# Kernel tuning notes

Measured on AMD Instinct MI355X. Metric: run time of the kernel, lower is better.

The kernel has to match this reference:

```python
import jax, jax.numpy as jnp
import numpy as np

NQ, NKV, D = 16, 2, 128
GROUPS = NQ // NKV
HID = 2048
SCALE = D ** -0.5
SLIDING_WINDOW = 32768
USE_WINDOW = True  # layer_idx 0 < max_window_layers 28
ROPE_THETA = 1e6


def rotate_half(x):
    h = x.shape[-1] // 2
    return jnp.concatenate([-x[..., h:], x[..., :h]], axis=-1)


def setup_inputs() -> dict:
    key = jax.random.key(0)
    ks = jax.random.split(key, 8)
    B, T = 1, 4096
    x = jax.random.normal(ks[0], (B, T, HID), dtype=jnp.float32)
    # Real RoPE tables (cos/sin over [T, D])
    inv_freq = 1.0 / (ROPE_THETA ** (np.arange(0, D, 2, dtype=np.float64) / D))
    freqs = np.outer(np.arange(T, dtype=np.float64), inv_freq)
    emb = np.concatenate([freqs, freqs], axis=-1)  # [T, D]
    cos = jnp.asarray(np.cos(emb), dtype=jnp.float32)
    sin = jnp.asarray(np.sin(emb), dtype=jnp.float32)
    std = 0.02
    wq = jax.random.normal(ks[1], (NQ * D, HID), dtype=jnp.float32) * std
    bq = jax.random.normal(ks[2], (NQ * D,), dtype=jnp.float32) * std
    wk = jax.random.normal(ks[3], (NKV * D, HID), dtype=jnp.float32) * std
    bk = jax.random.normal(ks[4], (NKV * D,), dtype=jnp.float32) * std
    wv = jax.random.normal(ks[5], (NKV * D, HID), dtype=jnp.float32) * std
    bv = jax.random.normal(ks[6], (NKV * D,), dtype=jnp.float32) * std
    wo = jax.random.normal(ks[7], (HID, NQ * D), dtype=jnp.float32) * std
    return {"x": x, "cos": cos, "sin": sin, "wq": wq, "bq": bq,
            "wk": wk, "bk": bk, "wv": wv, "bv": bv, "wo": wo}


def reference(x, cos, sin, wq, bq, wk, bk, wv, bv, wo):
    B, T, _ = x.shape
    # Projections -> [B, heads, T, D]
    q = (x @ wq.T + bq).reshape(B, T, NQ, D).transpose(0, 2, 1, 3)
    k = (x @ wk.T + bk).reshape(B, T, NKV, D).transpose(0, 2, 1, 3)
    v = (x @ wv.T + bv).reshape(B, T, NKV, D).transpose(0, 2, 1, 3)
    # RoPE
    c = cos[:T][None, None]  # [1,1,T,D]
    s = sin[:T][None, None]
    q = q * c + rotate_half(q) * s
    k = k * c + rotate_half(k) * s
    S = k.shape[2]  # no kv_cache -> S == T
    # GQA: group q heads over kv heads instead of repeat_interleave (same math)
    qg = q.reshape(B, NKV, GROUPS, T, D)
    attn = jnp.einsum('bkgtd,bksd->bkgts', qg, k) * SCALE  # [B,nkv,g,T,S]
    row = jnp.arange(T)[:, None]
    col = jnp.arange(S)[None, :]
    mask = jnp.where(col > row + (S - T), -jnp.inf, 0.0).astype(x.dtype)
    if USE_WINDOW and S > SLIDING_WINDOW:  # static shapes -> ok under jit
        mask = jnp.where(col < S - SLIDING_WINDOW, -jnp.inf, mask)
    attn = jax.nn.softmax(attn + mask[None, None, None], axis=-1)
    out = jnp.einsum('bkgts,bksd->bkgtd', attn, v)  # [B,nkv,g,T,D]
    out = out.reshape(B, NQ, T, D).transpose(0, 2, 1, 3).reshape(B, T, NQ * D)
    return out @ wo.T
```

## Files before the change

kernel.cpp:

```cpp
#include <hip/hip_runtime.h>
#include <hip/hip_bf16.h>
#include <stdint.h>

#define T_SEQ 4096
#define HID   2048
#define NQH   16
#define NKVH  2
#define DH    128
#define NQKV  2560
#define SCALE 0.08838834764831845f
#define QK_PRESCALE (0.08838834764831845f * 1.4426950408889634f)

typedef unsigned short u16;
typedef __attribute__((ext_vector_type(8))) short bf16x8;
typedef __attribute__((ext_vector_type(4))) float f32x4;

#define MFMA(a, b, c) __builtin_amdgcn_mfma_f32_16x16x32_bf16(a, b, c, 0, 0, 0)

static __device__ __forceinline__ u16 f2bf(float f) {
    union { float f; uint32_t u; } v; v.f = f;
    uint32_t r = v.u + 0x7fffu + ((v.u >> 16) & 1u);
    return (u16)(r >> 16);
}
static __device__ __forceinline__ float bf2f(u16 u) {
    union { uint32_t u; float f; } v; v.u = ((uint32_t)u) << 16;
    return v.f;
}

static __device__ __forceinline__ void gload_lds16(const void* g, void* l) {
    __builtin_amdgcn_global_load_lds((const __attribute__((address_space(1))) uint32_t*)g,
                                     (__attribute__((address_space(3))) uint32_t*)l,
                                     16, 0, 0);
}

__global__ void k_cvt_all(const float4* __restrict__ x,  const float4* __restrict__ wq,
                          const float4* __restrict__ wk, const float4* __restrict__ wv,
                          const float4* __restrict__ wo,
                          u16* __restrict__ x_bf, u16* __restrict__ wqkv_bf,
                          u16* __restrict__ wo_bf) {
    const int i = blockIdx.x * 256 + threadIdx.x;
    const float4* src; u16* dst; int off;
    if (i < 2097152)      { src = x;  dst = x_bf;              off = i; }
    else if (i < 3145728) { src = wq; dst = wqkv_bf;           off = i - 2097152; }
    else if (i < 3276800) { src = wk; dst = wqkv_bf + 4194304; off = i - 3145728; }
    else if (i < 3407872) { src = wv; dst = wqkv_bf + 4718592; off = i - 3276800; }
    else                  { src = wo; dst = wo_bf;             off = i - 3407872; }
    const float4 v = src[off];
    const uint64_t o = (uint64_t)f2bf(v.x) | ((uint64_t)f2bf(v.y) << 16) |
                       ((uint64_t)f2bf(v.z) << 32) | ((uint64_t)f2bf(v.w) << 48);
    *(uint64_t*)(dst + (size_t)off * 4) = o;
}

__global__ void k_bias(const float* __restrict__ bq, const float* __restrict__ bk,
                       const float* __restrict__ bv, float* __restrict__ out) {
    int i = blockIdx.x * 256 + threadIdx.x;
    float v = (i < 2048) ? bq[i] : (i < 2304 ? bk[i - 2048] : bv[i - 2304]);
    out[i] = v;
}

template <int OUT_BF16>
__global__ __launch_bounds__(256, 2) void k_gemm_bt(const u16* __restrict__ A,
                                                    const u16* __restrict__ B,
                                                    const float* __restrict__ bias,
                                                    void* __restrict__ Cout,
                                                    int M, int N, int K) {
    __shared__ u16 As[128 * 32];
    __shared__ u16 Bs[128 * 32];
    const int tid  = threadIdx.x;
    const int lane = tid & 63, w = tid >> 6;
    const int wr = w >> 1, wc = w & 1;
    const int lrow = lane & 15, lgrp = lane >> 4;
    const int m0 = blockIdx.x * 128, n0 = blockIdx.y * 128;

    f32x4 acc[4][4] = {};
    const int arow = tid >> 2, acol = (tid & 3) * 8;
    const u16* Abase = A + (size_t)(m0 + arow) * K + acol;
    const u16* Bbase = B + (size_t)(n0 + arow) * K + acol;

    for (int kk = 0; kk < K; kk += 32) {
        gload_lds16(Abase + kk,                   &As[tid * 8]);
        gload_lds16(Abase + kk + (size_t)64 * K,  &As[2048 + tid * 8]);
        gload_lds16(Bbase + kk,                   &Bs[tid * 8]);
        gload_lds16(Bbase + kk + (size_t)64 * K,  &Bs[2048 + tid * 8]);
        __syncthreads();
        bf16x8 af[4], bfv[4];
#pragma unroll
        for (int mb = 0; mb < 4; ++mb)
            af[mb] = *(const bf16x8*)&As[(wr * 64 + mb * 16 + lrow) * 32 + lgrp * 8];
#pragma unroll
        for (int nb = 0; nb < 4; ++nb)
            bfv[nb] = *(const bf16x8*)&Bs[(wc * 64 + nb * 16 + lrow) * 32 + lgrp * 8];
#pragma unroll
        for (int mb = 0; mb < 4; ++mb)
#pragma unroll
            for (int nb = 0; nb < 4; ++nb)
                acc[mb][nb] = MFMA(af[mb], bfv[nb], acc[mb][nb]);
        __syncthreads();
    }
#pragma unroll
    for (int mb = 0; mb < 4; ++mb)
#pragma unroll
        for (int nb = 0; nb < 4; ++nb) {
            const int col = n0 + wc * 64 + nb * 16 + lrow;
            const float bv_ = bias ? bias[col] : 0.f;
#pragma unroll
            for (int r = 0; r < 4; ++r) {
                const int row = m0 + wr * 64 + mb * 16 + lgrp * 4 + r;
                const float v = acc[mb][nb][r] + bv_;
                if (OUT_BF16) ((u16*)Cout)[(size_t)row * N + col] = f2bf(v);
                else          ((float*)Cout)[(size_t)row * N + col] = v;
            }
        }
}

__global__ void k_rope(const u16* __restrict__ qkv, const float* __restrict__ cosb,
                       const float* __restrict__ sinb, u16* __restrict__ Q,
                       u16* __restrict__ Kd, u16* __restrict__ VT) {
    const int n = blockIdx.x * 256 + threadIdx.x;
    const int t = blockIdx.y;
    const u16* row = qkv + (size_t)t * NQKV;
    if (n < 2304) {
        const int d = n & 127;
        const float x = bf2f(row[n]);
        const float p = bf2f(row[(d < 64) ? n + 64 : n - 64]);
        const float c = cosb[t * DH + d], s = sinb[t * DH + d];
        float val = (d < 64) ? (x * c - p * s) : (x * c + p * s);
        if (n < 2048) {
            const int h = n >> 7;
            Q[((size_t)h * T_SEQ + t) * DH + d] = f2bf(val * QK_PRESCALE);
        } else {
            const int kh = (n - 2048) >> 7;
            const int u = (d >> 3) ^ (t & 7);
            Kd[((size_t)kh * T_SEQ + t) * DH + u * 8 + (d & 7)] = f2bf(val);
        }
    } else {
        const int nv = n - 2304;
        const int kh = nv >> 7, d = nv & 127;
        const int kappa = t & 63;
        const int c = (kappa & 15) * 4 + (kappa >> 4);
        const int u = (c >> 3) ^ (d & 7);
        VT[((size_t)kh * DH + d) * T_SEQ + (t & ~63) + u * 8 + (c & 7)] = row[n];
    }
}

__global__ __launch_bounds__(256, 2) void k_attn(const u16* __restrict__ Q,
                                                 const u16* __restrict__ Kg,
                                                 const u16* __restrict__ VT,
                                                 u16* __restrict__ O) {
    __shared__ u16 Ks[2][64 * 128];
    __shared__ u16 VTs[64 * 128];
    __shared__ __align__(16) u16 Pb[4][16][72];
    const int tid  = threadIdx.x;
    const int lane = tid & 63, w = tid >> 6;
    const int lrow = lane & 15, lgrp = lane >> 4;
    const int g = blockIdx.x;
    const int h = g & 15, pp = g >> 4;
    const int kvh = h >> 3;

    const u16* Kbase = Kg + (size_t)kvh * T_SEQ * DH;
    const u16* Vbase = VT + (size_t)kvh * DH * T_SEQ;

    auto STAGE_K = [&](int buf, int it) {
        const u16* kg = Kbase + (size_t)(it * 64 + (tid >> 4)) * DH + (tid & 15) * 8;
#pragma unroll
        for (int c = 0; c < 4; ++c)
            gload_lds16(kg + (size_t)c * 16 * DH, &Ks[buf][c * 2048 + tid * 8]);
    };
    auto STAGE_V = [&](int it) {
        const u16* vg = Vbase + (size_t)(tid >> 3) * T_SEQ + it * 64 + (tid & 7) * 8;
#pragma unroll
        for (int c = 0; c < 4; ++c)
            gload_lds16(vg + (size_t)c * 32 * T_SEQ, &VTs[c * 2048 + tid * 8]);
    };

    for (int ph = 0; ph < 2; ++ph) {
        const int qt = ph ? pp : (63 - pp);
        const int q0 = qt * 64;
        const int qw = q0 + w * 16;

        bf16x8 aq[4];
#pragma unroll
        for (int kd = 0; kd < 4; ++kd)
            aq[kd] = *(const bf16x8*)&Q[((size_t)h * T_SEQ + qw + lrow) * DH +
                                        kd * 32 + lgrp * 8];

        f32x4 acc_o[8] = {};
        float m_s[4], l_s[4];
#pragma unroll
        for (int r = 0; r < 4; ++r) { m_s[r] = -1e30f; l_s[r] = 0.f; }

        STAGE_K(0, 0);
        STAGE_V(0);
        STAGE_K(1, 1);

        for (int it = 0; it <= qt; ++it) {
            const int cur = it & 1;
            if (it < qt) asm volatile("s_waitcnt vmcnt(4)" ::: "memory");
            else         asm volatile("s_waitcnt vmcnt(0)" ::: "memory");
            __builtin_amdgcn_s_barrier();
            const int kv0 = it * 64;

            f32x4 sacc[4] = {};
#pragma unroll
            for (int kd = 0; kd < 4; ++kd) {
                bf16x8 bk[4];
#pragma unroll
                for (int kvb = 0; kvb < 4; ++kvb)
                    bk[kvb] = *(const bf16x8*)&Ks[cur][(kvb * 16 + lrow) * 128 +
                                                      (((kd * 4 + lgrp) ^ (lrow & 7)) * 8)];
#pragma unroll
                for (int kvb = 0; kvb < 4; ++kvb)
                    sacc[kvb] = MFMA(aq[kd], bk[kvb], sacc[kvb]);
            }
            const bool needmask = (it == qt);
#pragma unroll
            for (int r = 0; r < 4; ++r) {
                float v[4];
#pragma unroll
                for (int kvb = 0; kvb < 4; ++kvb) v[kvb] = sacc[kvb][r];
                if (needmask) {
                    const int qrow = qw + lgrp * 4 + r;
#pragma unroll
                    for (int kvb = 0; kvb < 4; ++kvb)
                        if (kv0 + kvb * 16 + lrow > qrow) v[kvb] = -1e30f;
                }
                float pm = fmaxf(fmaxf(v[0], v[1]), fmaxf(v[2], v[3]));
#pragma unroll
                for (int off = 1; off < 16; off <<= 1)
                    pm = fmaxf(pm, __shfl_xor(pm, off));
                if (!__all(pm <= m_s[r] + 8.0f)) {
                    const float mo = m_s[r];
                    const float mn = fmaxf(mo, pm);
                    const float cc = exp2f(mo - mn);
                    l_s[r] *= cc;
#pragma unroll
                    for (int nb = 0; nb < 8; ++nb) acc_o[nb][r] *= cc;
                    m_s[r] = mn;
                }
                const float mm = m_s[r];
                float ps = 0.f;
#pragma unroll
                for (int kvb = 0; kvb < 4; ++kvb) {
                    v[kvb] = exp2f(v[kvb] - mm);
                    ps += v[kvb];
                }
                l_s[r] += ps;
                uint32_t pk0, pk1;
                asm("v_cvt_pk_bf16_f32 %0, %1, %2" : "=v"(pk0) : "v"(v[0]), "v"(v[1]));
                asm("v_cvt_pk_bf16_f32 %0, %1, %2" : "=v"(pk1) : "v"(v[2]), "v"(v[3]));
                *(uint2*)&Pb[w][lgrp * 4 + r][lrow * 4] = make_uint2(pk0, pk1);
            }
#pragma unroll
            for (int ks = 0; ks < 2; ++ks) {
                bf16x8 ap = *(const bf16x8*)&Pb[w][lrow][ks * 32 + lgrp * 8];
#pragma unroll
                for (int nb = 0; nb < 8; ++nb) {
                    bf16x8 bv = *(const bf16x8*)&VTs[(nb * 16 + lrow) * 64 +
                                                     (((ks * 4 + lgrp) ^ (lrow & 7)) * 8)];
                    acc_o[nb] = MFMA(ap, bv, acc_o[nb]);
                }
            }
            __builtin_amdgcn_s_barrier();
            if (it + 1 <= qt) {
                STAGE_V(it + 1);
                if (it + 2 <= qt) STAGE_K(cur, it + 2);
            }
        }

        float inv[4];
#pragma unroll
        for (int r = 0; r < 4; ++r) {
            float lv = l_s[r];
#pragma unroll
            for (int off = 1; off < 16; off <<= 1)
                lv += __shfl_xor(lv, off);
            inv[r] = 1.0f / lv;
        }
#pragma unroll
        for (int nb = 0; nb < 8; ++nb)
#pragma unroll
            for (int r = 0; r < 4; ++r) {
                const int row = qw + lgrp * 4 + r;
                const int col = h * DH + nb * 16 + lrow;
                O[(size_t)row * HID + col] = f2bf(acc_o[nb][r] * inv[r]);
            }
    }
}

extern "C" void kernel_launch(void* const* d_in, const int* in_sizes, int n_in,
                              void* d_out, int out_size, void* d_ws, size_t ws_size,
                              hipStream_t stream) {
    const float* x    = (const float*)d_in[0];
    const float* cosb = (const float*)d_in[1];
    const float* sinb = (const float*)d_in[2];
    const float* wq   = (const float*)d_in[3];
    const float* bq   = (const float*)d_in[4];
    const float* wk   = (const float*)d_in[5];
    const float* bk   = (const float*)d_in[6];
    const float* wv   = (const float*)d_in[7];
    const float* bv   = (const float*)d_in[8];
    const float* wo   = (const float*)d_in[9];
    float* out = (float*)d_out;

    char* ws = (char*)d_ws;
    u16*   x_bf    = (u16*)(ws);
    u16*   Qb      = (u16*)(ws);
    u16*   wqkv_bf = (u16*)(ws + 16777216);
    u16*   wo_bf   = (u16*)(ws + 27262976);
    float* bias    = (float*)(ws + 35651584);
    u16*   qkv     = (u16*)(ws + 35667968);
    u16*   Ob      = (u16*)(ws + 35667968);
    u16*   Kb      = (u16*)(ws + 56639488);
    u16*   VTb     = (u16*)(ws + 58736640);

    k_cvt_all<<<17408, 256, 0, stream>>>((const float4*)x, (const float4*)wq,
                                         (const float4*)wk, (const float4*)wv,
                                         (const float4*)wo, x_bf, wqkv_bf, wo_bf);
    k_bias<<<10, 256, 0, stream>>>(bq, bk, bv, bias);

    k_gemm_bt<1><<<dim3(32, 20), 256, 0, stream>>>(x_bf, wqkv_bf, bias, qkv, 4096, 2560, 2048);
    k_rope<<<dim3(10, 4096), 256, 0, stream>>>(qkv, cosb, sinb, Qb, Kb, VTb);
    k_attn<<<512, 256, 0, stream>>>(Qb, Kb, VTb, Ob);
    k_gemm_bt<0><<<dim3(32, 16), 256, 0, stream>>>(Ob, wo_bf, nullptr, out, 4096, 2048, 2048);
}
```

Before: 409.1 us.

## Compute transposed S in attention to keep P in registers, drop LDS round-trip

The QK^T MFMA now runs with operands swapped, so each lane holds scores for a single query row. That lets the row max and sum use only two cross-lane shuffles, and the bf16 P fragment is packed straight into registers for the PV MFMA with no staging through LDS. The V transpose permutation in the rope kernel is changed to match the new P register layout. The two-phase paired work per block is replaced by one query tile per block with twice as many blocks and a higher occupancy hint. The risks are load imbalance from dropping the causal pairing and register pressure at three blocks per CU.

```diff
diff --git a/kernel.cpp b/kernel.cpp
--- a/kernel.cpp
+++ b/kernel.cpp
@@ -8,7 +8,6 @@
 #define NKVH  2
 #define DH    128
 #define NQKV  2560
-#define SCALE 0.08838834764831845f
 #define QK_PRESCALE (0.08838834764831845f * 1.4426950408889634f)
 
 typedef unsigned short u16;
@@ -137,34 +136,35 @@
         const int nv = n - 2304;
         const int kh = nv >> 7, d = nv & 127;
         const int kappa = t & 63;
-        const int c = (kappa & 15) * 4 + (kappa >> 4);
+        const int c = (kappa & 0x20) | ((kappa & 0xC) << 1) | ((kappa & 0x10) >> 2) | (kappa & 3);
         const int u = (c >> 3) ^ (d & 7);
         VT[((size_t)kh * DH + d) * T_SEQ + (t & ~63) + u * 8 + (c & 7)] = row[n];
     }
 }
 
-__global__ __launch_bounds__(256, 2) void k_attn(const u16* __restrict__ Q,
+__global__ __launch_bounds__(256, 3) void k_attn(const u16* __restrict__ Q,
                                                  const u16* __restrict__ Kg,
                                                  const u16* __restrict__ VT,
                                                  u16* __restrict__ O) {
     __shared__ u16 Ks[2][64 * 128];
     __shared__ u16 VTs[64 * 128];
-    __shared__ __align__(16) u16 Pb[4][16][72];
     const int tid  = threadIdx.x;
     const int lane = tid & 63, w = tid >> 6;
-    const int lrow = lane & 15, lgrp = lane >> 4;
+    const int ql = lane & 15, kg = lane >> 4;
     const int g = blockIdx.x;
-    const int h = g & 15, pp = g >> 4;
+    const int h = g & 15, qt = 63 - (g >> 4);
     const int kvh = h >> 3;
+    const int q0 = qt * 64;
+    const int qw = q0 + w * 16;
 
     const u16* Kbase = Kg + (size_t)kvh * T_SEQ * DH;
     const u16* Vbase = VT + (size_t)kvh * DH * T_SEQ;
 
     auto STAGE_K = [&](int buf, int it) {
-        const u16* kg = Kbase + (size_t)(it * 64 + (tid >> 4)) * DH + (tid & 15) * 8;
+        const u16* kg_ = Kbase + (size_t)(it * 64 + (tid >> 4)) * DH + (tid & 15) * 8;
 #pragma unroll
         for (int c = 0; c < 4; ++c)
-            gload_lds16(kg + (size_t)c * 16 * DH, &Ks[buf][c * 2048 + tid * 8]);
+            gload_lds16(kg_ + (size_t)c * 16 * DH, &Ks[buf][c * 2048 + tid * 8]);
     };
     auto STAGE_V = [&](int it) {
         const u16* vg = Vbase + (size_t)(tid >> 3) * T_SEQ + it * 64 + (tid & 7) * 8;
@@ -173,117 +173,108 @@
             gload_lds16(vg + (size_t)c * 32 * T_SEQ, &VTs[c * 2048 + tid * 8]);
     };
 
-    for (int ph = 0; ph < 2; ++ph) {
-        const int qt = ph ? pp : (63 - pp);
-        const int q0 = qt * 64;
-        const int qw = q0 + w * 16;
-
-        bf16x8 aq[4];
-#pragma unroll
-        for (int kd = 0; kd < 4; ++kd)
-            aq[kd] = *(const bf16x8*)&Q[((size_t)h * T_SEQ + qw + lrow) * DH +
-                                        kd * 32 + lgrp * 8];
-
-        f32x4 acc_o[8] = {};
-        float m_s[4], l_s[4];
-#pragma unroll
-        for (int r = 0; r < 4; ++r) { m_s[r] = -1e30f; l_s[r] = 0.f; }
-
-        STAGE_K(0, 0);
-        STAGE_V(0);
-        STAGE_K(1, 1);
-
-        for (int it = 0; it <= qt; ++it) {
-            const int cur = it & 1;
-            if (it < qt) asm volatile("s_waitcnt vmcnt(4)" ::: "memory");
-            else         asm volatile("s_waitcnt vmcnt(0)" ::: "memory");
-            __builtin_amdgcn_s_barrier();
-            const int kv0 = it * 64;
-
-            f32x4 sacc[4] = {};
-#pragma unroll
-            for (int kd = 0; kd < 4; ++kd) {
-                bf16x8 bk[4];
-#pragma unroll
-                for (int kvb = 0; kvb < 4; ++kvb)
-                    bk[kvb] = *(const bf16x8*)&Ks[cur][(kvb * 16 + lrow) * 128 +
-                                                      (((kd * 4 + lgrp) ^ (lrow & 7)) * 8)];
-#pragma unroll
-                for (int kvb = 0; kvb < 4; ++kvb)
-                    sacc[kvb] = MFMA(aq[kd], bk[kvb], sacc[kvb]);
+    bf16x8 aq[4];
+#pragma unroll
+    for (int kd = 0; kd < 4; ++kd)
+        aq[kd] = *(const bf16x8*)&Q[((size_t)h * T_SEQ + qw + ql) * DH + kd * 32 + kg * 8];
+
+    f32x4 acc_o[8] = {};
+    float m_s = -1e30f, l_s = 0.f;
+
+    STAGE_K(0, 0);
+    STAGE_V(0);
+    STAGE_K(1, 1);
+
+    for (int it = 0; it <= qt; ++it) {
+        const int cur = it & 1;
+        if (it < qt) asm volatile("s_waitcnt vmcnt(4)" ::: "memory");
+        else         asm volatile("s_waitcnt vmcnt(0)" ::: "memory");
+        __builtin_amdgcn_s_barrier();
+        const int kv0 = it * 64;
+
+        f32x4 sacc[4] = {};
+#pragma unroll
+        for (int kd = 0; kd < 4; ++kd) {
+            bf16x8 bk[4];
+#pragma unroll
+            for (int kvb = 0; kvb < 4; ++kvb)
+                bk[kvb] = *(const bf16x8*)&Ks[cur][(kvb * 16 + ql) * 128 +
+                                                  (((kd * 4 + kg) ^ (ql & 7)) * 8)];
+#pragma unroll
+            for (int kvb = 0; kvb < 4; ++kvb)
+                sacc[kvb] = MFMA(bk[kvb], aq[kd], sacc[kvb]);
+        }
+        if (it == qt) {
+            const int thr = qw + ql - kv0 - kg * 4;
+#pragma unroll
+            for (int kvb = 0; kvb < 4; ++kvb)
+#pragma unroll
+                for (int r = 0; r < 4; ++r)
+                    if (kvb * 16 + r > thr) sacc[kvb][r] = -1e30f;
+        }
+        float pm = -1e30f;
+#pragma unroll
+        for (int kvb = 0; kvb < 4; ++kvb)
+#pragma unroll
+            for (int r = 0; r < 4; ++r) pm = fmaxf(pm, sacc[kvb][r]);
+        pm = fmaxf(pm, __shfl_xor(pm, 16));
+        pm = fmaxf(pm, __shfl_xor(pm, 32));
+        if (!__all(pm <= m_s + 8.0f)) {
+            const float mn = fmaxf(m_s, pm);
+            const float cc = exp2f(m_s - mn);
+            l_s *= cc;
+#pragma unroll
+            for (int nb = 0; nb < 8; ++nb)
+#pragma unroll
+                for (int r = 0; r < 4; ++r) acc_o[nb][r] *= cc;
+            m_s = mn;
+        }
+        float ps = 0.f;
+#pragma unroll
+        for (int kvb = 0; kvb < 4; ++kvb)
+#pragma unroll
+            for (int r = 0; r < 4; ++r) {
+                sacc[kvb][r] = exp2f(sacc[kvb][r] - m_s);
+                ps += sacc[kvb][r];
             }
-            const bool needmask = (it == qt);
-#pragma unroll
-            for (int r = 0; r < 4; ++r) {
-                float v[4];
-#pragma unroll
-                for (int kvb = 0; kvb < 4; ++kvb) v[kvb] = sacc[kvb][r];
-                if (needmask) {
-                    const int qrow = qw + lgrp * 4 + r;
-#pragma unroll
-                    for (int kvb = 0; kvb < 4; ++kvb)
-                        if (kv0 + kvb * 16 + lrow > qrow) v[kvb] = -1e30f;
-                }
-                float pm = fmaxf(fmaxf(v[0], v[1]), fmaxf(v[2], v[3]));
-#pragma unroll
-                for (int off = 1; off < 16; off <<= 1)
-                    pm = fmaxf(pm, __shfl_xor(pm, off));
-                if (!__all(pm <= m_s[r] + 8.0f)) {
-                    const float mo = m_s[r];
-                    const float mn = fmaxf(mo, pm);
-                    const float cc = exp2f(mo - mn);
-                    l_s[r] *= cc;
-#pragma unroll
-                    for (int nb = 0; nb < 8; ++nb) acc_o[nb][r] *= cc;
-                    m_s[r] = mn;
-                }
-                const float mm = m_s[r];
-                float ps = 0.f;
-#pragma unroll
-                for (int kvb = 0; kvb < 4; ++kvb) {
-                    v[kvb] = exp2f(v[kvb] - mm);
-                    ps += v[kvb];
-                }
-                l_s[r] += ps;
-                uint32_t pk0, pk1;
-                asm("v_cvt_pk_bf16_f32 %0, %1, %2" : "=v"(pk0) : "v"(v[0]), "v"(v[1]));
-                asm("v_cvt_pk_bf16_f32 %0, %1, %2" : "=v"(pk1) : "v"(v[2]), "v"(v[3]));
-                *(uint2*)&Pb[w][lgrp * 4 + r][lrow * 4] = make_uint2(pk0, pk1);
+        l_s += ps;
+        union { bf16x8 v; uint32_t u[4]; } pb[2];
+#pragma unroll
+        for (int kvb = 0; kvb < 4; ++kvb) {
+            uint32_t lo, hi;
+            asm("v_cvt_pk_bf16_f32 %0, %1, %2" : "=v"(lo) : "v"(sacc[kvb][0]), "v"(sacc[kvb][1]));
+            asm("v_cvt_pk_bf16_f32 %0, %1, %2" : "=v"(hi) : "v"(sacc[kvb][2]), "v"(sacc[kvb][3]));
+            pb[kvb >> 1].u[(kvb & 1) * 2]     = lo;
+            pb[kvb >> 1].u[(kvb & 1) * 2 + 1] = hi;
+        }
+#pragma unroll
+        for (int ks = 0; ks < 2; ++ks)
+#pragma unroll
+            for (int nb = 0; nb < 8; ++nb) {
+                bf16x8 bv = *(const bf16x8*)&VTs[(nb * 16 + ql) * 64 +
+                                                 (((ks * 4 + kg) ^ (ql & 7)) * 8)];
+                acc_o[nb] = MFMA(bv, pb[ks].v, acc_o[nb]);
             }
-#pragma unroll
-            for (int ks = 0; ks < 2; ++ks) {
-                bf16x8 ap = *(const bf16x8*)&Pb[w][lrow][ks * 32 + lgrp * 8];
-#pragma unroll
-                for (int nb = 0; nb < 8; ++nb) {
-                    bf16x8 bv = *(const bf16x8*)&VTs[(nb * 16 + lrow) * 64 +
-                                                     (((ks * 4 + lgrp) ^ (lrow & 7)) * 8)];
-                    acc_o[nb] = MFMA(ap, bv, acc_o[nb]);
-                }
-            }
-            __builtin_amdgcn_s_barrier();
-            if (it + 1 <= qt) {
-                STAGE_V(it + 1);
-                if (it + 2 <= qt) STAGE_K(cur, it + 2);
-            }
-        }
-
-        float inv[4];
-#pragma unroll
-        for (int r = 0; r < 4; ++r) {
-            float lv = l_s[r];
-#pragma unroll
-            for (int off = 1; off < 16; off <<= 1)
-                lv += __shfl_xor(lv, off);
-            inv[r] = 1.0f / lv;
-        }
-#pragma unroll
-        for (int nb = 0; nb < 8; ++nb)
-#pragma unroll
-            for (int r = 0; r < 4; ++r) {
-                const int row = qw + lgrp * 4 + r;
-                const int col = h * DH + nb * 16 + lrow;
-                O[(size_t)row * HID + col] = f2bf(acc_o[nb][r] * inv[r]);
-            }
+        __builtin_amdgcn_s_barrier();
+        if (it + 1 <= qt) {
+            STAGE_V(it + 1);
+            if (it + 2 <= qt) STAGE_K(cur, it + 2);
+        }
+    }
+
+    float lv = l_s;
+    lv += __shfl_xor(lv, 16);
+    lv += __shfl_xor(lv, 32);
+    const float inv = 1.0f / lv;
+    const size_t orow = (size_t)(qw + ql) * HID + h * DH;
+#pragma unroll
+    for (int nb = 0; nb < 8; ++nb) {
+        uint32_t a, b;
+        const float o0 = acc_o[nb][0] * inv, o1 = acc_o[nb][1] * inv;
+        const float o2 = acc_o[nb][2] * inv, o3 = acc_o[nb][3] * inv;
+        asm("v_cvt_pk_bf16_f32 %0, %1, %2" : "=v"(a) : "v"(o0), "v"(o1));
+        asm("v_cvt_pk_bf16_f32 %0, %1, %2" : "=v"(b) : "v"(o2), "v"(o3));
+        *(uint2*)&O[orow + nb * 16 + kg * 4] = make_uint2(a, b);
     }
 }
 
@@ -320,6 +311,6 @@
 
     k_gemm_bt<1><<<dim3(32, 20), 256, 0, stream>>>(x_bf, wqkv_bf, bias, qkv, 4096, 2560, 2048);
     k_rope<<<dim3(10, 4096), 256, 0, stream>>>(qkv, cosb, sinb, Qb, Kb, VTb);
-    k_attn<<<512, 256, 0, stream>>>(Qb, Kb, VTb, Ob);
+    k_attn<<<1024, 256, 0, stream>>>(Qb, Kb, VTb, Ob);
     k_gemm_bt<0><<<dim3(32, 16), 256, 0, stream>>>(Ob, wo_bf, nullptr, out, 4096, 2048, 2048);
 }
```

After: 359.2 us. 12.2% less time.
